# Performance work log

Hardware: AMD Instinct MI355X
Metric: run time of the kernel (lower is better)

Reference implementation:

```python
import jax, jax.numpy as jnp
import numpy as np
from jax.ops import segment_sum, segment_max

B, NPG, EPG = 2048, 32, 64          # graphs per drug, nodes/graph, edges/graph
N, E = B * NPG, B * EPG
FIN, EIN = 70, 6
HID, H, C = 128, 2, 64              # hidd_dim, conv heads, head_out_feats
NBLK, NCLASS = 4, 2
CAH, CAD = 8, 128                   # co-attention heads, dim_head


def _elu(x):
    return jnp.where(x > 0, x, jnp.expm1(x))


def _ln_graph(x, batch, w, b):
    # PyG LayerNorm(mode='graph'): normalize over all nodes+channels of each graph.
    cnt = jnp.float32(NPG * x.shape[1])  # all graphs have NPG nodes
    mean = segment_sum(x.sum(-1), batch, num_segments=B) / cnt
    xc = x - mean[batch][:, None]
    var = segment_sum((xc * xc).sum(-1), batch, num_segments=B) / cnt
    return xc * jax.lax.rsqrt(var + 1e-5)[batch][:, None] * w + b


def _ln(x, w, b):
    mu = x.mean(-1, keepdims=True)
    v = ((x - mu) ** 2).mean(-1, keepdims=True)
    return (x - mu) * jax.lax.rsqrt(v + 1e-5) * w + b


def _tconv(x, src, dst, ea, Wq, bq, Wk, bk, Wv, bv, We, Ws, bs):
    # PyG TransformerConv: edge-attention gather -> softmax over incoming edges -> scatter.
    q = (x @ Wq + bq).reshape(-1, H, C)
    k = (x @ Wk + bk).reshape(-1, H, C)
    v = (x @ Wv + bv).reshape(-1, H, C)
    e = (ea @ We).reshape(-1, H, C)
    kj = k[src] + e                                   # [E,H,C]
    a = (q[dst] * kj).sum(-1) * (C ** -0.5)           # [E,H]
    amax = segment_max(a, dst, num_segments=N)
    a = jnp.exp(a - amax[dst])
    a = a / (segment_sum(a, dst, num_segments=N)[dst] + 1e-16)
    out = segment_sum((v[src] + e) * a[:, :, None], dst, num_segments=N)
    return out.reshape(-1, H * C) + x @ Ws + bs       # root/skip connection


def _pool(x, src, dst, ea, batch, ebatch, w_rel, b_rel, w_root, W_re, b_re):
    # SAGPooling(min_score=-1): GraphConv score, per-graph softmax, all nodes kept,
    # then score-weighted global_add_pool; edge_attr pooled per graph and merged.
    agg = segment_sum(x[src], dst, num_segments=N)    # GraphConv 'add' aggregation
    score = agg @ w_rel + b_rel + x @ w_root          # [N]
    smax = segment_max(score, batch, num_segments=B)
    sexp = jnp.exp(score - smax[batch])
    score = sexp / (segment_sum(sexp, batch, num_segments=B)[batch] + 1e-16)
    g = segment_sum(x * score[:, None], batch, num_segments=B)      # [B,HID]
    ge = _elu(segment_sum(ea, ebatch, num_segments=B) @ W_re + b_re)
    g = g * ge
    return g / jnp.maximum(jnp.linalg.norm(g, axis=1, keepdims=True), 1e-12)


def _coattn(qx, kvx, lw, lb, Wq, Wkv, Wo):
    qx = _ln(qx, lw, lb)
    kvx = _ln(kvx, lw, lb)
    b, n = qx.shape[0], qx.shape[1]
    q = (qx @ Wq).reshape(b, n, CAH, CAD).transpose(0, 2, 1, 3)
    k, v = jnp.split(kvx @ Wkv, 2, axis=-1)
    k = k.reshape(b, n, CAH, CAD).transpose(0, 2, 1, 3)
    v = v.reshape(b, n, CAH, CAD).transpose(0, 2, 1, 3)
    attn = jax.nn.softmax(jnp.einsum('bhnd,bhmd->bhnm', q, k) * (CAD ** -0.5), axis=-1)
    o = jnp.einsum('bhnm,bhmd->bhnd', attn, v).transpose(0, 2, 1, 3).reshape(b, n, CAH * CAD)
    return o @ Wo


def setup_inputs() -> dict:
    key = jax.random.key(0)
    ks = iter(jax.random.split(key, 64))

    def nrm(shape, fan):
        return jax.random.normal(next(ks), shape, jnp.float32) * (fan ** -0.5)

    inp = {}
    inp['x1'] = jax.random.normal(next(ks), (N, FIN), jnp.float32)
    inp['x2'] = jax.random.normal(next(ks), (N, FIN), jnp.float32)
    inp['ea1'] = jax.random.normal(next(ks), (E, EIN), jnp.float32)
    inp['ea2'] = jax.random.normal(next(ks), (E, EIN), jnp.float32)
    inp['W_node'] = nrm((FIN, HID), FIN); inp['b_node'] = jnp.zeros((HID,), jnp.float32)
    inp['W_edge'] = nrm((EIN, 64), EIN); inp['b_edge'] = jnp.zeros((64,), jnp.float32)
    inp['ln0_w'] = jnp.ones((HID,), jnp.float32); inp['ln0_b'] = jnp.zeros((HID,), jnp.float32)
    inp['Wq'] = nrm((NBLK, 2, HID, HID), HID); inp['bq'] = jnp.zeros((NBLK, 2, HID), jnp.float32)
    inp['Wk'] = nrm((NBLK, 2, HID, HID), HID); inp['bk'] = jnp.zeros((NBLK, 2, HID), jnp.float32)
    inp['Wv'] = nrm((NBLK, 2, HID, HID), HID); inp['bv'] = jnp.zeros((NBLK, 2, HID), jnp.float32)
    inp['We'] = nrm((NBLK, 2, 64, HID), 64)
    inp['Ws'] = nrm((NBLK, 2, HID, HID), HID); inp['bs'] = jnp.zeros((NBLK, 2, HID), jnp.float32)
    inp['Wup'] = nrm((NBLK, 2, 64, 64), 64); inp['bup'] = jnp.zeros((NBLK, 2, 64), jnp.float32)
    inp['lnw'] = jnp.ones((NBLK, 2, HID), jnp.float32); inp['lnb'] = jnp.zeros((NBLK, 2, HID), jnp.float32)
    inp['w_rel'] = nrm((HID,), HID); inp['b_rel'] = jnp.zeros((), jnp.float32)
    inp['w_root'] = nrm((HID,), HID)
    inp['W_re'] = nrm((64, HID), 64); inp['b_re'] = jnp.zeros((HID,), jnp.float32)
    inp['ca_lw'] = jnp.ones((HID,), jnp.float32); inp['ca_lb'] = jnp.zeros((HID,), jnp.float32)
    inp['Wq_ca'] = nrm((HID, CAH * CAD), HID)
    inp['Wkv_ca'] = nrm((HID, 2 * CAH * CAD), HID)
    inp['Wo_ca'] = nrm((CAH * CAD, HID), CAH * CAD)
    inp['W_merge'] = nrm((NBLK * NBLK, NCLASS), NBLK * NBLK)
    inp['b_merge'] = jnp.zeros((NCLASS,), jnp.float32)
    off = jnp.repeat(jnp.arange(B, dtype=jnp.int32) * NPG, EPG)
    inp['edge_index1'] = jax.random.randint(next(ks), (2, E), 0, NPG, jnp.int32) + off[None, :]
    inp['edge_index2'] = jax.random.randint(next(ks), (2, E), 0, NPG, jnp.int32) + off[None, :]
    inp['batch1'] = jnp.repeat(jnp.arange(B, dtype=jnp.int32), NPG)
    inp['batch2'] = jnp.repeat(jnp.arange(B, dtype=jnp.int32), NPG)
    inp['ebatch1'] = jnp.repeat(jnp.arange(B, dtype=jnp.int32), EPG)
    inp['ebatch2'] = jnp.repeat(jnp.arange(B, dtype=jnp.int32), EPG)
    return inp


def reference(x1, x2, ea1, ea2, W_node, b_node, W_edge, b_edge, ln0_w, ln0_b,
              Wq, bq, Wk, bk, Wv, bv, We, Ws, bs, Wup, bup, lnw, lnb,
              w_rel, b_rel, w_root, W_re, b_re, ca_lw, ca_lb, Wq_ca, Wkv_ca, Wo_ca,
              W_merge, b_merge, edge_index1, edge_index2, batch1, batch2, ebatch1, ebatch2):
    s1, d1 = edge_index1[0], edge_index1[1]
    s2, d2 = edge_index2[0], edge_index2[1]
    x1 = _elu(_ln_graph(x1 @ W_node + b_node, batch1, ln0_w, ln0_b))
    x2 = _elu(_ln_graph(x2 @ W_node + b_node, batch2, ln0_w, ln0_b))
    ea1 = _elu(ea1 @ W_edge + b_edge)
    ea2 = _elu(ea2 @ W_edge + b_edge)

    def block(i, x, ea, src, dst, batch):
        x = _tconv(x, src, dst, ea, Wq[i, 0], bq[i, 0], Wk[i, 0], bk[i, 0],
                   Wv[i, 0], bv[i, 0], We[i, 0], Ws[i, 0], bs[i, 0])
        x = _elu(_ln_graph(x, batch, lnw[i, 0], lnb[i, 0]))
        ea = _elu(ea @ Wup[i, 0] + bup[i, 0])
        x = _tconv(x, src, dst, ea, Wq[i, 1], bq[i, 1], Wk[i, 1], bk[i, 1],
                   Wv[i, 1], bv[i, 1], We[i, 1], Ws[i, 1], bs[i, 1])
        ea_next = ea @ Wup[i, 1] + bup[i, 1]
        x = _elu(_ln_graph(x, batch, lnw[i, 1], lnb[i, 1]))
        return x, _elu(ea_next)

    hs, ts = [], []
    for i in range(NBLK):
        x1, ea1 = block(i, x1, ea1, s1, d1, batch1)
        x2, ea2 = block(i, x2, ea2, s2, d2, batch2)
        hs.append(_pool(x1, s1, d1, ea1, batch1, ebatch1, w_rel, b_rel, w_root, W_re, b_re))
        ts.append(_pool(x2, s2, d2, ea2, batch2, ebatch2, w_rel, b_rel, w_root, W_re, b_re))
    rh = jnp.stack(hs, 1)  # [B, NBLK, HID]
    rt = jnp.stack(ts, 1)
    ha = _coattn(rh, rt, ca_lw, ca_lb, Wq_ca, Wkv_ca, Wo_ca)
    ta = _coattn(rt, rh, ca_lw, ca_lb, Wq_ca, Wkv_ca, Wo_ca)
    m = jnp.einsum('bnd,bmd->bnm', ha, ta).reshape(ha.shape[0], NBLK * NBLK)
    return jax.nn.softmax(m @ W_merge + b_merge, axis=-1)
```

## Files before the change

kernel.cpp:

```cpp
#include <hip/hip_runtime.h>
#include <cstddef>
#include <cstdint>

#define NGRAPH 2048
#define NPG    32
#define EPG    64
#define NNODE  (NGRAPH*NPG)
#define NEDGE  (NGRAPH*EPG)
#define FINDIM 70
#define EINDIM 6
#define HID    128
#define NBLK   4
#define CAH    8
#define CAD    128
#define ES     68
#define XS     132

typedef __attribute__((ext_vector_type(8))) short bf16x8_t;
typedef __attribute__((ext_vector_type(4))) float f32x4;
typedef unsigned short ushortb;

#define MF3(accv, Ah_, Al_, Bh_, Bl_)                                          \
  accv = __builtin_amdgcn_mfma_f32_16x16x32_bf16(Ah_, Bh_, accv, 0, 0, 0);     \
  accv = __builtin_amdgcn_mfma_f32_16x16x32_bf16(Ah_, Bl_, accv, 0, 0, 0);     \
  accv = __builtin_amdgcn_mfma_f32_16x16x32_bf16(Al_, Bh_, accv, 0, 0, 0);

__device__ inline void split8(const float* p, bf16x8_t& h, bf16x8_t& l) {
  float4 v0 = *(const float4*)p, v1 = *(const float4*)(p + 4);
  float vv[8] = {v0.x, v0.y, v0.z, v0.w, v1.x, v1.y, v1.z, v1.w};
#pragma unroll
  for (int j = 0; j < 8; j++) {
    unsigned u = __builtin_bit_cast(unsigned, vv[j]);
    h[j] = (short)(u >> 16);
    float r = vv[j] - __builtin_bit_cast(float, u & 0xFFFF0000u);
    l[j] = (short)(__builtin_bit_cast(unsigned, r) >> 16);
  }
}

template<bool BIAS, bool ELU>
__global__ __launch_bounds__(256) void gemm_kernel(
    const float* __restrict__ A, const float* __restrict__ W,
    const float* __restrict__ bias, float* __restrict__ C,
    int M, int K, int Nc) {
  __shared__ float As[8][64];
  __shared__ float Bs[8][65];
  const int bm = blockIdx.y * 64, bn = blockIdx.x * 64;
  const int tid = threadIdx.x;
  const int tr = tid >> 4, tc = tid & 15;
  float acc[4][4];
// ... 162 lines not shown
  const int g = blockIdx.x, t = threadIdx.x;
  const float* xg = in + (size_t)g * NPG * HID;
  float* og = out + (size_t)g * NPG * HID;
  float vals[16];
  float s = 0.f, ss = 0.f;
#pragma unroll
  for (int i = 0; i < 16; i++) {
    float v = xg[t + i * 256];
    vals[i] = v; s += v; ss += v * v;
  }
  __shared__ float ws0[4], ws1[4];
  for (int off = 32; off > 0; off >>= 1) { s += __shfl_down(s, off); ss += __shfl_down(ss, off); }
  int wid = t >> 6, lane = t & 63;
  if (lane == 0) { ws0[wid] = s; ws1[wid] = ss; }
  __syncthreads();
  if (t == 0) {
    float S = 0.f, SS = 0.f;
    for (int i = 0; i < 4; i++) { S += ws0[i]; SS += ws1[i]; }
    float mean = S / 4096.f;
    float var = SS / 4096.f - mean * mean;
    ws0[0] = mean; ws1[0] = rsqrtf(var + 1e-5f);
  }
  __syncthreads();
  float mean = ws0[0], inv = ws1[0];
#pragma unroll
  for (int i = 0; i < 16; i++) {
    int idx = t + i * 256;
    int ch = idx & 127;
    float y = (vals[i] - mean) * inv * w[ch] + b[ch];
    og[idx] = y > 0.f ? y : expm1f(y);
  }
}

template<bool POOL>
__global__ __launch_bounds__(256, 4) void mega_kernel(
    float* __restrict__ xb, float* __restrict__ ea,
    const ushortb* __restrict__ Wqkvh, const ushortb* __restrict__ Wqkvl,
    const ushortb* __restrict__ Wsh, const ushortb* __restrict__ Wsl,
    const ushortb* __restrict__ WeTh, const ushortb* __restrict__ WeTl,
    const ushortb* __restrict__ Wuph, const ushortb* __restrict__ Wupl,
    const float* __restrict__ bqkv_, const float* __restrict__ bs_,
    const float* __restrict__ bup_, const float* __restrict__ lnw_,
    const float* __restrict__ lnb_,
    const float* __restrict__ w_rel, const float* __restrict__ b_rel,
    const float* __restrict__ w_root, const float* __restrict__ W_re,
    const float* __restrict__ b_re, float* __restrict__ outp, int blk,
    const int* __restrict__ src, const int* __restrict__ dst) {
  const int g = blockIdx.x, t = threadIdx.x;
  const int lane = t & 63, w = t >> 6, l16 = lane & 15, lk = lane >> 4;
  __shared__ float el[EPG * ES];
  __shared__ float qs2[NPG * ES];
  __shared__ float ks2[NPG * ES];
  __shared__ unsigned char lists[NPG * EPG];
  __shared__ int deg_[NPG];
  __shared__ int sl[EPG], dl[EPG];
  __shared__ float alE[128];
  __shared__ float red0[NPG], red1[NPG];

  if (t < EPG) { sl[t] = src[g * EPG + t] - g * NPG; dl[t] = dst[g * EPG + t] - g * NPG; }
  if (t < NPG) {
    int c = 0;
    for (int e = 0; e < EPG; e++)
      if (dl[e] == t) lists[t * EPG + (c++)] = (unsigned char)e;
    deg_[t] = c;
  }

  bf16x8_t xh[2][4], xL[2][4];
#pragma unroll
  for (int m = 0; m < 2; m++)
#pragma unroll
    for (int kc = 0; kc < 4; kc++)
      split8(xb + ((size_t)g * NPG + m * 16 + l16) * HID + kc * 32 + lk * 8,
             xh[m][kc], xL[m][kc]);
  const float* eag = ea + ((size_t)g * EPG + w * 16 + l16) * 64;

  float accH0[8], accH1[8];
#pragma unroll
  for (int c = 0; c < 8; c++) { accH0[c] = 0.f; accH1[c] = 0.f; }

  auto proj = [&](int baseN, float* dstL) {
    f32x4 pa0 = (f32x4)0.f, pa1 = (f32x4)0.f;
#pragma unroll
    for (int kc = 0; kc < 4; kc++) {
      size_t o = (size_t)(baseN + w * 16 + l16) * HID + kc * 32 + lk * 8;
      bf16x8_t bh = *(const bf16x8_t*)(Wqkvh + o);
      bf16x8_t bl = *(const bf16x8_t*)(Wqkvl + o);
      MF3(pa0, xh[0][kc], xL[0][kc], bh, bl);
      MF3(pa1, xh[1][kc], xL[1][kc], bh, bl);
    }
    float bv = bqkv_[baseN + w * 16 + l16];
#pragma unroll
    for (int r = 0; r < 4; r++) {
      dstL[(lk * 4 + r) * ES + w * 16 + l16] = pa0[r] + bv;
      dstL[(16 + lk * 4 + r) * ES + w * 16 + l16] = pa1[r] + bv;
    }
  };

  auto head = [&](const int h, float (&acc8)[8]) {
    {
      bf16x8_t ea0h, ea0l, ea1h, ea1l;
      split8(eag + lk * 8, ea0h, ea0l);
      split8(eag + 32 + lk * 8, ea1h, ea1l);
#pragma unroll 1
      for (int n = 0; n < 4; n++) {
        f32x4 acc = (f32x4)0.f;
        size_t o0 = (size_t)(h * 64 + n * 16 + l16) * 64 + lk * 8;
        bf16x8_t bh0 = *(const bf16x8_t*)(WeTh + o0);
        bf16x8_t bl0 = *(const bf16x8_t*)(WeTl + o0);
        MF3(acc, ea0h, ea0l, bh0, bl0);
        bf16x8_t bh1 = *(const bf16x8_t*)(WeTh + o0 + 32);
        bf16x8_t bl1 = *(const bf16x8_t*)(WeTl + o0 + 32);
        MF3(acc, ea1h, ea1l, bh1, bl1);
#pragma unroll
        for (int r = 0; r < 4; r++)
          el[(w * 16 + lk * 4 + r) * ES + n * 16 + l16] = acc[r];
      }
    }
    proj(h * 64, qs2);
    proj(128 + h * 64, ks2);
    __syncthreads();
    {
      const int e2 = t >> 2, part = t & 3;
      const float* qp = qs2 + dl[e2] * ES + part * 16;
      const float* kp = ks2 + sl[e2] * ES + part * 16;
      const float* ep = el + e2 * ES + part * 16;
      float s = 0.f;
#pragma unroll
      for (int c = 0; c < 16; c += 4) {
        float4 qv = *(const float4*)(qp + c);
        float4 kv = *(const float4*)(kp + c);
        float4 ev = *(const float4*)(ep + c);
        s += qv.x * (kv.x + ev.x) + qv.y * (kv.y + ev.y) +
             qv.z * (kv.z + ev.z) + qv.w * (kv.w + ev.w);
      }
      s += __shfl_xor(s, 1);
      s += __shfl_xor(s, 2);
      if (part == 0) alE[e2] = s * 0.125f;
    }
    __syncthreads();
    f32x4 va0 = (f32x4)0.f, va1 = (f32x4)0.f;
#pragma unroll
    for (int kc = 0; kc < 4; kc++) {
      size_t o = (size_t)(256 + h * 64 + w * 16 + l16) * HID + kc * 32 + lk * 8;
      bf16x8_t bh = *(const bf16x8_t*)(Wqkvh + o);
      bf16x8_t bl = *(const bf16x8_t*)(Wqkvl + o);
      MF3(va0, xh[0][kc], xL[0][kc], bh, bl);
      MF3(va1, xh[1][kc], xL[1][kc], bh, bl);
    }
    {
      const int n = t >> 3, part = t & 7;
      float su = 0.f;
#pragma unroll 1
      for (int i = 0; i < 8; i++) {
        int e2 = part * 8 + i;
        if (dl[e2] == n) su += expf(alE[e2]);
      }
      su += __shfl_xor(su, 1);
      su += __shfl_xor(su, 2);
      su += __shfl_xor(su, 4);
      if (part == 0) red1[n] = su;
    }
    {
      float bv = bqkv_[256 + h * 64 + w * 16 + l16];
#pragma unroll
      for (int r = 0; r < 4; r++) {
        ks2[(lk * 4 + r) * ES + w * 16 + l16] = va0[r] + bv;
        ks2[(16 + lk * 4 + r) * ES + w * 16 + l16] = va1[r] + bv;
      }
    }
    __syncthreads();
    {
      const int n = t >> 3, cg = t & 7;
      const float inv = 1.f / (red1[n] + 1e-16f);
      const int dg = deg_[n];
      for (int i = 0; i < dg; i++) {
        const int e2 = lists[n * EPG + i];
        const float a = expf(alE[e2]) * inv;
        const float* vp = ks2 + sl[e2] * ES + cg * 8;
        const float* ep = el + e2 * ES + cg * 8;
        float4 v0 = *(const float4*)vp, v1 = *(const float4*)(vp + 4);
        float4 e0 = *(const float4*)ep, e1 = *(const float4*)(ep + 4);
        acc8[0] += a * (v0.x + e0.x); acc8[1] += a * (v0.y + e0.y);
        acc8[2] += a * (v0.z + e0.z); acc8[3] += a * (v0.w + e0.w);
        acc8[4] += a * (v1.x + e1.x); acc8[5] += a * (v1.y + e1.y);
        acc8[6] += a * (v1.z + e1.z); acc8[7] += a * (v1.w + e1.w);
      }
    }
    __syncthreads();
  };

  head(0, accH0);
  head(1, accH1);

  {
#pragma unroll
    for (int n = 0; n < 2; n++) {
      f32x4 sa0 = (f32x4)0.f, sa1 = (f32x4)0.f;
#pragma unroll
      for (int kc = 0; kc < 4; kc++) {
        size_t o = (size_t)(w * 32 + n * 16 + l16) * HID + kc * 32 + lk * 8;
        bf16x8_t bh = *(const bf16x8_t*)(Wsh + o);
        bf16x8_t bl = *(const bf16x8_t*)(Wsl + o);
        MF3(sa0, xh[0][kc], xL[0][kc], bh, bl);
        MF3(sa1, xh[1][kc], xL[1][kc], bh, bl);
      }
      int col = w * 32 + n * 16 + l16;
      float bv = bs_[col];
#pragma unroll
      for (int r = 0; r < 4; r++) {
        el[(lk * 4 + r) * XS + col] = sa0[r] + bv;
        el[(16 + lk * 4 + r) * XS + col] = sa1[r] + bv;
      }
    }
  }
  f32x4 ua[4];
  {
    bf16x8_t ea0h, ea0l, ea1h, ea1l;
    split8(eag + lk * 8, ea0h, ea0l);
    split8(eag + 32 + lk * 8, ea1h, ea1l);
#pragma unroll
    for (int n = 0; n < 4; n++) {
      f32x4 acc = (f32x4)0.f;
      size_t o0 = (size_t)(n * 16 + l16) * 64 + lk * 8;
      bf16x8_t bh0 = *(const bf16x8_t*)(Wuph + o0);
      bf16x8_t bl0 = *(const bf16x8_t*)(Wupl + o0);
      MF3(acc, ea0h, ea0l, bh0, bl0);
      bf16x8_t bh1 = *(const bf16x8_t*)(Wuph + o0 + 32);
      bf16x8_t bl1 = *(const bf16x8_t*)(Wupl + o0 + 32);
      MF3(acc, ea1h, ea1l, bh1, bl1);
      int col = n * 16 + l16;
      float bv = bup_[col];
#pragma unroll
      for (int r = 0; r < 4; r++) {
        float y = acc[r] + bv;
        y = y > 0.f ? y : expm1f(y);
        ua[n][r] = y;
        ea[((size_t)g * EPG + w * 16 + lk * 4 + r) * 64 + col] = y;
      }
    }
  }
  __syncthreads();
  {
    const int n = t >> 3, cg = t & 7;
    float v16[16];
#pragma unroll
    for (int c = 0; c < 8; c++) {
      v16[c] = accH0[c] + el[n * XS + cg * 8 + c];
      v16[8 + c] = accH1[c] + el[n * XS + 64 + cg * 8 + c];
    }
    float s = 0.f, ss = 0.f;
#pragma unroll
    for (int j = 0; j < 16; j++) { s += v16[j]; ss += v16[j] * v16[j]; }
    for (int o2 = 32; o2 > 0; o2 >>= 1) { s += __shfl_down(s, o2); ss += __shfl_down(ss, o2); }
    if (lane == 0) { red0[w] = s; red1[w] = ss; }
    __syncthreads();
    if (t == 0) {
      float S = red0[0] + red0[1] + red0[2] + red0[3];
      float SS = red1[0] + red1[1] + red1[2] + red1[3];
      float mean = S / 4096.f;
      float var = SS / 4096.f - mean * mean;
      red0[0] = mean; red1[0] = rsqrtf(var + 1e-5f);
    }
    __syncthreads();
    float mean = red0[0], inv = red1[0];
    float* xg = xb + (size_t)g * NPG * HID;
#pragma unroll
    for (int hh = 0; hh < 2; hh++)
#pragma unroll
      for (int c = 0; c < 8; c++) {
        int col = hh * 64 + cg * 8 + c;
        float y = (v16[hh * 8 + c] - mean) * inv * lnw_[col] + lnb_[col];
        y = y > 0.f ? y : expm1f(y);
        xg[n * HID + col] = y;
        el[n * XS + col] = y;
      }
  }

  if constexpr (POOL) {
    __syncthreads();
    {
#pragma unroll
      for (int n = 0; n < 4; n++) {
        float s = ua[n][0] + ua[n][1] + ua[n][2] + ua[n][3];
        s += __shfl_xor(s, 16);
        s += __shfl_xor(s, 32);
        if (lk == 0) qs2[w * 64 + n * 16 + l16] = s;
      }
      const int n = t >> 3, part = t & 7;
      float s = 0.f;
      for (int c = part * 16; c < part * 16 + 16; c++)
        s += el[n * XS + c] * w_root[c];
      const int dg = deg_[n];
      for (int i = 0; i < dg; i++) {
        int sn = sl[lists[n * EPG + i]];
        for (int c = part * 16; c < part * 16 + 16; c++)
          s += el[sn * XS + c] * w_rel[c];
      }
      s += __shfl_xor(s, 1);
      s += __shfl_xor(s, 2);
      s += __shfl_xor(s, 4);
      if (part == 0) alE[n] = s + b_rel[0];
    }
    __syncthreads();
    if (t < 64)
      alE[64 + t] = qs2[t] + qs2[64 + t] + qs2[128 + t] + qs2[192 + t];
    if (t >= 128 && t < 160) {
      int n = t - 128;
      float sc = alE[n];
      float m = sc;
      for (int o2 = 1; o2 <= 16; o2 <<= 1) m = fmaxf(m, __shfl_xor(m, o2));
      float e = expf(sc - m);
      float su = e;
      for (int o2 = 1; o2 <= 16; o2 <<= 1) su += __shfl_xor(su, o2);
      alE[n] = e / (su + 1e-16f);
    }
    __syncthreads();
    if (t < HID) {
      const int ch = t;
      float gv = 0.f;
      for (int n = 0; n < NPG; n++) gv += alE[n] * el[n * XS + ch];
      float s2 = b_re[ch];
      for (int k2 = 0; k2 < 64; k2++) s2 += alE[64 + k2] * W_re[k2 * HID + ch];
      s2 = s2 > 0.f ? s2 : expm1f(s2);
      float gl = gv * s2;
      el[4224 + ch] = gl;
      float sq = gl * gl;
      for (int o2 = 32; o2 > 0; o2 >>= 1) sq += __shfl_down(sq, o2);
      if (lane == 0) red0[w] = sq;
    }
    __syncthreads();
    if (t == 0) red1[0] = fmaxf(sqrtf(red0[0] + red0[1]), 1e-12f);
    __syncthreads();
    if (t < HID)
      outp[((size_t)g * NBLK + blk) * HID + t] = el[4224 + t] / red1[0];
  }
}

__global__ void ln_row_kernel(const float* __restrict__ in, float* __restrict__ out,
                              const float* __restrict__ w, const float* __restrict__ b) {
  const int r = blockIdx.x, t = threadIdx.x;
  float v = in[(size_t)r * HID + t];
  float s = v, ss = v * v;
  for (int off = 32; off > 0; off >>= 1) { s += __shfl_down(s, off); ss += __shfl_down(ss, off); }
  __shared__ float s0[2], s1[2];
  if ((t & 63) == 0) { s0[t >> 6] = s; s1[t >> 6] = ss; }
  __syncthreads();
  float S = s0[0] + s0[1], SS = s1[0] + s1[1];
  float mean = S / 128.f, var = SS / 128.f - mean * mean;
  out[(size_t)r * HID + t] = (v - mean) * rsqrtf(var + 1e-5f) * w[t] + b[t];
}

__global__ void coattn_kernel(const float* __restrict__ qb, const float* __restrict__ kvb,
                              float* __restrict__ ob) {
  const int bh = blockIdx.x, b = bh >> 3, h = bh & 7, t = threadIdx.x;
  __shared__ float attn[4][4];
  __shared__ float red[64];
  const int pair = t >> 2, part = t & 3;
  const int n = pair >> 2, m = pair & 3;
  const float* qp = qb + ((size_t)(b * 4 + n) * (CAH * CAD)) + h * CAD;
  const float* kp = kvb + ((size_t)(b * 4 + m) * (2 * CAH * CAD)) + h * CAD;
  float s = 0.f;
  for (int d = part * 32; d < part * 32 + 32; d++) s += qp[d] * kp[d];
  red[t] = s;
  __syncthreads();
  if (t < 16) {
    float sc = (red[t * 4] + red[t * 4 + 1] + red[t * 4 + 2] + red[t * 4 + 3]) * 0.08838834764831845f;
    attn[t >> 2][t & 3] = sc;
// ... 110 lines not shown
  ushortb* Wkvh = allocb(262144);    ushortb* Wkvl = allocb(262144);
  ushortb* Woh = allocb(131072);     ushortb* Wol = allocb(131072);
  float* bqkv = alloc(8 * 384);
  if (off > ws_size) return;

  float* qc  = xb;
  float* kvc = big;
  float* oc  = ea;

  auto convw = [&](const float* s, ushortb* h, ushortb* l, int K, int N, int B,
                   int dstN, int nOff) {
    int tot = B * K * N;
    convw_kernel<<<(tot + 255) / 256, 256, 0, stream>>>(s, h, l, K, N, tot, dstN, nOff);
  };
  convw(Wq, Wqkvh, Wqkvl, 128, 128, 8, 384, 0);
  convw(Wk, Wqkvh, Wqkvl, 128, 128, 8, 384, 128);
  convw(Wv, Wqkvh, Wqkvl, 128, 128, 8, 384, 256);
  convw(Wskip, Wsh, Wsl, 128, 128, 8, 128, 0);
  convw(Wup, Wuph, Wupl, 64, 64, 8, 64, 0);
  convw(We, WeTh, WeTl, 64, 128, 8, 128, 0);
  convw(Wq_ca, Wqcah, Wqcal, 128, 1024, 1, 1024, 0);
  convw(Wkv_ca, Wkvh, Wkvl, 128, 2048, 1, 2048, 0);
  convw(Wo_ca, Woh, Wol, 1024, 128, 1, 128, 0);
  bcat_kernel<<<(8 * 384 + 255) / 256, 256, 0, stream>>>(bq, bk, bv, bqkv);

  for (int d2 = 0; d2 < 2; ++d2) {
    const int* src = ei[d2];
    const int* dst = ei[d2] + NEDGE;
    run_gemm(xin[d2], W_node, b_node, xb, NNODE, FINDIM, HID, false, stream);
    ln_graph_elu_kernel<<<NGRAPH, 256, 0, stream>>>(xb, xb, ln0_w, ln0_b);
    run_gemm(eain[d2], W_edge, b_edge, ea, NEDGE, EINDIM, 64, true, stream);
    float* outp = d2 == 0 ? hs : ts;
    for (int i = 0; i < NBLK; ++i) {
      int pi0 = i * 2, pi1 = i * 2 + 1;
      mega_kernel<false><<<NGRAPH, 256, 0, stream>>>(
          xb, ea,
          Wqkvh + (size_t)pi0 * 49152, Wqkvl + (size_t)pi0 * 49152,
          Wsh + (size_t)pi0 * 16384, Wsl + (size_t)pi0 * 16384,
          WeTh + (size_t)pi0 * 8192, WeTl + (size_t)pi0 * 8192,
          Wuph + (size_t)pi0 * 4096, Wupl + (size_t)pi0 * 4096,
          bqkv + pi0 * 384, bs + pi0 * 128, bup + pi0 * 64,
          lnw + pi0 * 128, lnb + pi0 * 128,
          w_rel, b_rel, w_root, W_re, b_re, nullptr, 0, src, dst);
      mega_kernel<true><<<NGRAPH, 256, 0, stream>>>(
          xb, ea,
          Wqkvh + (size_t)pi1 * 49152, Wqkvl + (size_t)pi1 * 49152,
          Wsh + (size_t)pi1 * 16384, Wsl + (size_t)pi1 * 16384,
          WeTh + (size_t)pi1 * 8192, WeTl + (size_t)pi1 * 8192,
          Wuph + (size_t)pi1 * 4096, Wupl + (size_t)pi1 * 4096,
          bqkv + pi1 * 384, bs + pi1 * 128, bup + pi1 * 64,
          lnw + pi1 * 128, lnb + pi1 * 128,
          w_rel, b_rel, w_root, W_re, b_re, outp, i, src, dst);
    }
  }

  ln_row_kernel<<<NGRAPH * NBLK, 128, 0, stream>>>(hs, rhn, ca_lw, ca_lb);
  ln_row_kernel<<<NGRAPH * NBLK, 128, 0, stream>>>(ts, rtn, ca_lw, ca_lb);
  run_mf8(rhn, Wqcah, Wqcal, qc, NGRAPH * NBLK, 128, 1024, stream);
  run_mf8(rtn, Wkvh, Wkvl, kvc, NGRAPH * NBLK, 128, 2048, stream);
  coattn_kernel<<<NGRAPH * CAH, 64, 0, stream>>>(qc, kvc, oc);
  run_mf8(oc, Woh, Wol, hab, NGRAPH * NBLK, 1024, 128, stream);
  run_mf8(rtn, Wqcah, Wqcal, qc, NGRAPH * NBLK, 128, 1024, stream);
  run_mf8(rhn, Wkvh, Wkvl, kvc, NGRAPH * NBLK, 128, 2048, stream);
  coattn_kernel<<<NGRAPH * CAH, 64, 0, stream>>>(qc, kvc, oc);
  run_mf8(oc, Woh, Wol, tab, NGRAPH * NBLK, 1024, 128, stream);

  final_kernel<<<NGRAPH, 64, 0, stream>>>(hab, tab, W_merge, b_merge, out);
}
```

Before: 3.234 ms.

## Fuse both TransformerConv layers of each block into one per-graph kernel

Merges the two per-layer mega kernels of a block into a single launch that loops over both layers. The intermediate node features and updated edge features stay in shared memory and registers between layers instead of being written to and re-read from global memory. It also saves the edge-tile setup and a kernel launch per block. In exchange the kernel holds more live state and its launch bound drops from 4 to 3 blocks per CU, which may reduce occupancy.

```diff
diff --git a/kernel.cpp b/kernel.cpp
--- a/kernel.cpp
+++ b/kernel.cpp
@@ -15,6 +15,7 @@
 #define CAD    128
 #define ES     68
 #define XS     132
+#define TS     66
 
 typedef __attribute__((ext_vector_type(8))) short bf16x8_t;
 typedef __attribute__((ext_vector_type(4))) float f32x4;
@@ -243,16 +244,15 @@
   }
 }
 
-template<bool POOL>
-__global__ __launch_bounds__(256, 4) void mega_kernel(
+__global__ __launch_bounds__(256, 3) void mega2_kernel(
     float* __restrict__ xb, float* __restrict__ ea,
-    const ushortb* __restrict__ Wqkvh, const ushortb* __restrict__ Wqkvl,
-    const ushortb* __restrict__ Wsh, const ushortb* __restrict__ Wsl,
-    const ushortb* __restrict__ WeTh, const ushortb* __restrict__ WeTl,
-    const ushortb* __restrict__ Wuph, const ushortb* __restrict__ Wupl,
-    const float* __restrict__ bqkv_, const float* __restrict__ bs_,
-    const float* __restrict__ bup_, const float* __restrict__ lnw_,
-    const float* __restrict__ lnb_,
+    const ushortb* __restrict__ Wqkvh0, const ushortb* __restrict__ Wqkvl0,
+    const ushortb* __restrict__ Wsh0, const ushortb* __restrict__ Wsl0,
+    const ushortb* __restrict__ WeTh0, const ushortb* __restrict__ WeTl0,
+    const ushortb* __restrict__ Wuph0, const ushortb* __restrict__ Wupl0,
+    const float* __restrict__ bqkv0, const float* __restrict__ bs0,
+    const float* __restrict__ bup0, const float* __restrict__ lnw0,
+    const float* __restrict__ lnb0,
     const float* __restrict__ w_rel, const float* __restrict__ b_rel,
     const float* __restrict__ w_root, const float* __restrict__ W_re,
     const float* __restrict__ b_re, float* __restrict__ outp, int blk,
@@ -260,13 +260,14 @@
   const int g = blockIdx.x, t = threadIdx.x;
   const int lane = t & 63, w = t >> 6, l16 = lane & 15, lk = lane >> 4;
   __shared__ float el[EPG * ES];
-  __shared__ float qs2[NPG * ES];
-  __shared__ float ks2[NPG * ES];
+  __shared__ float qks[2 * NPG * ES];
   __shared__ unsigned char lists[NPG * EPG];
   __shared__ int deg_[NPG];
   __shared__ int sl[EPG], dl[EPG];
   __shared__ float alE[128];
   __shared__ float red0[NPG], red1[NPG];
+  float* qs2 = qks;
+  float* ks2 = qks + NPG * ES;
 
   if (t < EPG) { sl[t] = src[g * EPG + t] - g * NPG; dl[t] = dst[g * EPG + t] - g * NPG; }
   if (t < NPG) {
@@ -283,267 +284,295 @@
     for (int kc = 0; kc < 4; kc++)
       split8(xb + ((size_t)g * NPG + m * 16 + l16) * HID + kc * 32 + lk * 8,
              xh[m][kc], xL[m][kc]);
-  const float* eag = ea + ((size_t)g * EPG + w * 16 + l16) * 64;
-
-  float accH0[8], accH1[8];
-#pragma unroll
-  for (int c = 0; c < 8; c++) { accH0[c] = 0.f; accH1[c] = 0.f; }
-
-  auto proj = [&](int baseN, float* dstL) {
-    f32x4 pa0 = (f32x4)0.f, pa1 = (f32x4)0.f;
-#pragma unroll
-    for (int kc = 0; kc < 4; kc++) {
-      size_t o = (size_t)(baseN + w * 16 + l16) * HID + kc * 32 + lk * 8;
-      bf16x8_t bh = *(const bf16x8_t*)(Wqkvh + o);
-      bf16x8_t bl = *(const bf16x8_t*)(Wqkvl + o);
-      MF3(pa0, xh[0][kc], xL[0][kc], bh, bl);
-      MF3(pa1, xh[1][kc], xL[1][kc], bh, bl);
-    }
-    float bv = bqkv_[baseN + w * 16 + l16];
-#pragma unroll
-    for (int r = 0; r < 4; r++) {
-      dstL[(lk * 4 + r) * ES + w * 16 + l16] = pa0[r] + bv;
-      dstL[(16 + lk * 4 + r) * ES + w * 16 + l16] = pa1[r] + bv;
-    }
-  };
-
-  auto head = [&](const int h, float (&acc8)[8]) {
+  bf16x8_t efh[2], efl[2];
+  {
+    const float* eag = ea + ((size_t)g * EPG + w * 16 + l16) * 64;
+    split8(eag + lk * 8, efh[0], efl[0]);
+    split8(eag + 32 + lk * 8, efh[1], efl[1]);
+  }
+
+  for (int half = 0; half < 2; ++half) {
+    const ushortb* Wqkvh = Wqkvh0 + half * 49152;
+    const ushortb* Wqkvl = Wqkvl0 + half * 49152;
+    const ushortb* Wsh = Wsh0 + half * 16384;
+    const ushortb* Wsl = Wsl0 + half * 16384;
+    const ushortb* WeTh = WeTh0 + half * 8192;
+    const ushortb* WeTl = WeTl0 + half * 8192;
+    const ushortb* Wuph = Wuph0 + half * 4096;
+    const ushortb* Wupl = Wupl0 + half * 4096;
+    const float* bqkv_ = bqkv0 + half * 384;
+    const float* bs_ = bs0 + half * 128;
+    const float* bup_ = bup0 + half * 64;
+    const float* lnw_ = lnw0 + half * 128;
+    const float* lnb_ = lnb0 + half * 128;
+
+    float accH0[8], accH1[8];
+#pragma unroll
+    for (int c = 0; c < 8; c++) { accH0[c] = 0.f; accH1[c] = 0.f; }
+
+    auto proj = [&](int baseN, float* dstL) {
+      f32x4 pa0 = (f32x4)0.f, pa1 = (f32x4)0.f;
+#pragma unroll
+      for (int kc = 0; kc < 4; kc++) {
+        size_t o = (size_t)(baseN + w * 16 + l16) * HID + kc * 32 + lk * 8;
+        bf16x8_t bh = *(const bf16x8_t*)(Wqkvh + o);
+        bf16x8_t bl = *(const bf16x8_t*)(Wqkvl + o);
+        MF3(pa0, xh[0][kc], xL[0][kc], bh, bl);
+        MF3(pa1, xh[1][kc], xL[1][kc], bh, bl);
+      }
+      float bv = bqkv_[baseN + w * 16 + l16];
+#pragma unroll
+      for (int r = 0; r < 4; r++) {
+        dstL[(lk * 4 + r) * ES + w * 16 + l16] = pa0[r] + bv;
+        dstL[(16 + lk * 4 + r) * ES + w * 16 + l16] = pa1[r] + bv;
+      }
+    };
+
+    auto head = [&](const int h, float (&acc8)[8]) {
+      {
+#pragma unroll 1
+        for (int n = 0; n < 4; n++) {
+          f32x4 acc = (f32x4)0.f;
+          size_t o0 = (size_t)(h * 64 + n * 16 + l16) * 64 + lk * 8;
+          bf16x8_t bh0 = *(const bf16x8_t*)(WeTh + o0);
+          bf16x8_t bl0 = *(const bf16x8_t*)(WeTl + o0);
+          MF3(acc, efh[0], efl[0], bh0, bl0);
+          bf16x8_t bh1 = *(const bf16x8_t*)(WeTh + o0 + 32);
+          bf16x8_t bl1 = *(const bf16x8_t*)(WeTl + o0 + 32);
+          MF3(acc, efh[1], efl[1], bh1, bl1);
+#pragma unroll
+          for (int r = 0; r < 4; r++)
+            el[(w * 16 + lk * 4 + r) * ES + n * 16 + l16] = acc[r];
+        }
+      }
+      proj(h * 64, qs2);
+      proj(128 + h * 64, ks2);
+      __syncthreads();
+      {
+        const int e2 = t >> 2, part = t & 3;
+        const float* qp = qs2 + dl[e2] * ES + part * 16;
+        const float* kp = ks2 + sl[e2] * ES + part * 16;
+        const float* ep = el + e2 * ES + part * 16;
+        float s = 0.f;
+#pragma unroll
+        for (int c = 0; c < 16; c += 4) {
+          float4 qv = *(const float4*)(qp + c);
+          float4 kv = *(const float4*)(kp + c);
+          float4 ev = *(const float4*)(ep + c);
+          s += qv.x * (kv.x + ev.x) + qv.y * (kv.y + ev.y) +
+               qv.z * (kv.z + ev.z) + qv.w * (kv.w + ev.w);
+        }
+        s += __shfl_xor(s, 1);
+        s += __shfl_xor(s, 2);
+        if (part == 0) alE[e2] = s * 0.125f;
+      }
+      __syncthreads();
+      f32x4 va0 = (f32x4)0.f, va1 = (f32x4)0.f;
+#pragma unroll
+      for (int kc = 0; kc < 4; kc++) {
+        size_t o = (size_t)(256 + h * 64 + w * 16 + l16) * HID + kc * 32 + lk * 8;
+        bf16x8_t bh = *(const bf16x8_t*)(Wqkvh + o);
+        bf16x8_t bl = *(const bf16x8_t*)(Wqkvl + o);
+        MF3(va0, xh[0][kc], xL[0][kc], bh, bl);
+        MF3(va1, xh[1][kc], xL[1][kc], bh, bl);
+      }
+      {
+        const int n = t >> 3, part = t & 7;
+        float su = 0.f;
+#pragma unroll 1
+        for (int i = 0; i < 8; i++) {
+          int e2 = part * 8 + i;
+          if (dl[e2] == n) su += expf(alE[e2]);
+        }
+        su += __shfl_xor(su, 1);
+        su += __shfl_xor(su, 2);
+        su += __shfl_xor(su, 4);
+        if (part == 0) red1[n] = su;
+      }
+      {
+        float bv = bqkv_[256 + h * 64 + w * 16 + l16];
+#pragma unroll
+        for (int r = 0; r < 4; r++) {
+          ks2[(lk * 4 + r) * ES + w * 16 + l16] = va0[r] + bv;
+          ks2[(16 + lk * 4 + r) * ES + w * 16 + l16] = va1[r] + bv;
+        }
+      }
+      __syncthreads();
+      {
+        const int n = t >> 3, cg = t & 7;
+        const float inv = 1.f / (red1[n] + 1e-16f);
+        const int dg = deg_[n];
+        for (int i = 0; i < dg; i++) {
+          const int e2 = lists[n * EPG + i];
+          const float a = expf(alE[e2]) * inv;
+          const float* vp = ks2 + sl[e2] * ES + cg * 8;
+          const float* ep = el + e2 * ES + cg * 8;
+          float4 v0 = *(const float4*)vp, v1 = *(const float4*)(vp + 4);
+          float4 e0 = *(const float4*)ep, e1 = *(const float4*)(ep + 4);
+          acc8[0] += a * (v0.x + e0.x); acc8[1] += a * (v0.y + e0.y);
+          acc8[2] += a * (v0.z + e0.z); acc8[3] += a * (v0.w + e0.w);
+          acc8[4] += a * (v1.x + e1.x); acc8[5] += a * (v1.y + e1.y);
+          acc8[6] += a * (v1.z + e1.z); acc8[7] += a * (v1.w + e1.w);
+        }
+      }
+      __syncthreads();
+    };
+
+    head(0, accH0);
+    head(1, accH1);
+
     {
-      bf16x8_t ea0h, ea0l, ea1h, ea1l;
-      split8(eag + lk * 8, ea0h, ea0l);
-      split8(eag + 32 + lk * 8, ea1h, ea1l);
-#pragma unroll 1
+#pragma unroll
+      for (int n = 0; n < 2; n++) {
+        f32x4 sa0 = (f32x4)0.f, sa1 = (f32x4)0.f;
+#pragma unroll
+        for (int kc = 0; kc < 4; kc++) {
+          size_t o = (size_t)(w * 32 + n * 16 + l16) * HID + kc * 32 + lk * 8;
+          bf16x8_t bh = *(const bf16x8_t*)(Wsh + o);
+          bf16x8_t bl = *(const bf16x8_t*)(Wsl + o);
+          MF3(sa0, xh[0][kc], xL[0][kc], bh, bl);
+          MF3(sa1, xh[1][kc], xL[1][kc], bh, bl);
+        }
+        int col = w * 32 + n * 16 + l16;
+        float bv = bs_[col];
+#pragma unroll
+        for (int r = 0; r < 4; r++) {
+          el[(lk * 4 + r) * XS + col] = sa0[r] + bv;
+          el[(16 + lk * 4 + r) * XS + col] = sa1[r] + bv;
+        }
+      }
+    }
+    f32x4 ua[4];
+    {
+#pragma unroll
       for (int n = 0; n < 4; n++) {
         f32x4 acc = (f32x4)0.f;
-        size_t o0 = (size_t)(h * 64 + n * 16 + l16) * 64 + lk * 8;
-        bf16x8_t bh0 = *(const bf16x8_t*)(WeTh + o0);
-        bf16x8_t bl0 = *(const bf16x8_t*)(WeTl + o0);
-        MF3(acc, ea0h, ea0l, bh0, bl0);
-        bf16x8_t bh1 = *(const bf16x8_t*)(WeTh + o0 + 32);
-        bf16x8_t bl1 = *(const bf16x8_t*)(WeTl + o0 + 32);
-        MF3(acc, ea1h, ea1l, bh1, bl1);
-#pragma unroll
-        for (int r = 0; r < 4; r++)
-          el[(w * 16 + lk * 4 + r) * ES + n * 16 + l16] = acc[r];
-      }
-    }
-    proj(h * 64, qs2);
-    proj(128 + h * 64, ks2);
-    __syncthreads();
-    {
-      const int e2 = t >> 2, part = t & 3;
-      const float* qp = qs2 + dl[e2] * ES + part * 16;
-      const float* kp = ks2 + sl[e2] * ES + part * 16;
-      const float* ep = el + e2 * ES + part * 16;
-      float s = 0.f;
-#pragma unroll
-      for (int c = 0; c < 16; c += 4) {
-        float4 qv = *(const float4*)(qp + c);
-        float4 kv = *(const float4*)(kp + c);
-        float4 ev = *(const float4*)(ep + c);
-        s += qv.x * (kv.x + ev.x) + qv.y * (kv.y + ev.y) +
-             qv.z * (kv.z + ev.z) + qv.w * (kv.w + ev.w);
-      }
-      s += __shfl_xor(s, 1);
-      s += __shfl_xor(s, 2);
-      if (part == 0) alE[e2] = s * 0.125f;
-    }
-    __syncthreads();
-    f32x4 va0 = (f32x4)0.f, va1 = (f32x4)0.f;
-#pragma unroll
-    for (int kc = 0; kc < 4; kc++) {
-      size_t o = (size_t)(256 + h * 64 + w * 16 + l16) * HID + kc * 32 + lk * 8;
-      bf16x8_t bh = *(const bf16x8_t*)(Wqkvh + o);
-      bf16x8_t bl = *(const bf16x8_t*)(Wqkvl + o);
-      MF3(va0, xh[0][kc], xL[0][kc], bh, bl);
-      MF3(va1, xh[1][kc], xL[1][kc], bh, bl);
-    }
-    {
-      const int n = t >> 3, part = t & 7;
-      float su = 0.f;
-#pragma unroll 1
-      for (int i = 0; i < 8; i++) {
-        int e2 = part * 8 + i;
-        if (dl[e2] == n) su += expf(alE[e2]);
-      }
-      su += __shfl_xor(su, 1);
-      su += __shfl_xor(su, 2);
-      su += __shfl_xor(su, 4);
-      if (part == 0) red1[n] = su;
-    }
-    {
-      float bv = bqkv_[256 + h * 64 + w * 16 + l16];
-#pragma unroll
-      for (int r = 0; r < 4; r++) {
-        ks2[(lk * 4 + r) * ES + w * 16 + l16] = va0[r] + bv;
-        ks2[(16 + lk * 4 + r) * ES + w * 16 + l16] = va1[r] + bv;
+        size_t o0 = (size_t)(n * 16 + l16) * 64 + lk * 8;
+        bf16x8_t bh0 = *(const bf16x8_t*)(Wuph + o0);
+        bf16x8_t bl0 = *(const bf16x8_t*)(Wupl + o0);
+        MF3(acc, efh[0], efl[0], bh0, bl0);
+        bf16x8_t bh1 = *(const bf16x8_t*)(Wuph + o0 + 32);
+        bf16x8_t bl1 = *(const bf16x8_t*)(Wupl + o0 + 32);
+        MF3(acc, efh[1], efl[1], bh1, bl1);
+        int col = n * 16 + l16;
+        float bv = bup_[col];
+#pragma unroll
+        for (int r = 0; r < 4; r++) {
+          float y = acc[r] + bv;
+          y = y > 0.f ? y : expm1f(y);
+          ua[n][r] = y;
+          if (half == 0)
+            qks[(w * 16 + lk * 4 + r) * TS + col] = y;
+          else
+            ea[((size_t)g * EPG + w * 16 + lk * 4 + r) * 64 + col] = y;
+        }
       }
     }
     __syncthreads();
     {
       const int n = t >> 3, cg = t & 7;
-      const float inv = 1.f / (red1[n] + 1e-16f);
-      const int dg = deg_[n];
-      for (int i = 0; i < dg; i++) {
-        const int e2 = lists[n * EPG + i];
-        const float a = expf(alE[e2]) * inv;
-        const float* vp = ks2 + sl[e2] * ES + cg * 8;
-        const float* ep = el + e2 * ES + cg * 8;
-        float4 v0 = *(const float4*)vp, v1 = *(const float4*)(vp + 4);
-        float4 e0 = *(const float4*)ep, e1 = *(const float4*)(ep + 4);
-        acc8[0] += a * (v0.x + e0.x); acc8[1] += a * (v0.y + e0.y);
-        acc8[2] += a * (v0.z + e0.z); acc8[3] += a * (v0.w + e0.w);
-        acc8[4] += a * (v1.x + e1.x); acc8[5] += a * (v1.y + e1.y);
-        acc8[6] += a * (v1.z + e1.z); acc8[7] += a * (v1.w + e1.w);
-      }
-    }
-    __syncthreads();
-  };
-
-  head(0, accH0);
-  head(1, accH1);
-
-  {
-#pragma unroll
-    for (int n = 0; n < 2; n++) {
-      f32x4 sa0 = (f32x4)0.f, sa1 = (f32x4)0.f;
-#pragma unroll
-      for (int kc = 0; kc < 4; kc++) {
-        size_t o = (size_t)(w * 32 + n * 16 + l16) * HID + kc * 32 + lk * 8;
-        bf16x8_t bh = *(const bf16x8_t*)(Wsh + o);
-        bf16x8_t bl = *(const bf16x8_t*)(Wsl + o);
-        MF3(sa0, xh[0][kc], xL[0][kc], bh, bl);
-        MF3(sa1, xh[1][kc], xL[1][kc], bh, bl);
-      }
-      int col = w * 32 + n * 16 + l16;
-      float bv = bs_[col];
-#pragma unroll
-      for (int r = 0; r < 4; r++) {
-        el[(lk * 4 + r) * XS + col] = sa0[r] + bv;
-        el[(16 + lk * 4 + r) * XS + col] = sa1[r] + bv;
-      }
-    }
-  }
-  f32x4 ua[4];
-  {
-    bf16x8_t ea0h, ea0l, ea1h, ea1l;
-    split8(eag + lk * 8, ea0h, ea0l);
-    split8(eag + 32 + lk * 8, ea1h, ea1l);
-#pragma unroll
-    for (int n = 0; n < 4; n++) {
-      f32x4 acc = (f32x4)0.f;
-      size_t o0 = (size_t)(n * 16 + l16) * 64 + lk * 8;
-      bf16x8_t bh0 = *(const bf16x8_t*)(Wuph + o0);
-      bf16x8_t bl0 = *(const bf16x8_t*)(Wupl + o0);
-      MF3(acc, ea0h, ea0l, bh0, bl0);
-      bf16x8_t bh1 = *(const bf16x8_t*)(Wuph + o0 + 32);
-      bf16x8_t bl1 = *(const bf16x8_t*)(Wupl + o0 + 32);
-      MF3(acc, ea1h, ea1l, bh1, bl1);
-      int col = n * 16 + l16;
-      float bv = bup_[col];
-#pragma unroll
-      for (int r = 0; r < 4; r++) {
-        float y = acc[r] + bv;
-        y = y > 0.f ? y : expm1f(y);
-        ua[n][r] = y;
-        ea[((size_t)g * EPG + w * 16 + lk * 4 + r) * 64 + col] = y;
-      }
-    }
-  }
-  __syncthreads();
-  {
-    const int n = t >> 3, cg = t & 7;
-    float v16[16];
-#pragma unroll
-    for (int c = 0; c < 8; c++) {
-      v16[c] = accH0[c] + el[n * XS + cg * 8 + c];
-      v16[8 + c] = accH1[c] + el[n * XS + 64 + cg * 8 + c];
-    }
-    float s = 0.f, ss = 0.f;
-#pragma unroll
-    for (int j = 0; j < 16; j++) { s += v16[j]; ss += v16[j] * v16[j]; }
-    for (int o2 = 32; o2 > 0; o2 >>= 1) { s += __shfl_down(s, o2); ss += __shfl_down(ss, o2); }
-    if (lane == 0) { red0[w] = s; red1[w] = ss; }
-    __syncthreads();
-    if (t == 0) {
-      float S = red0[0] + red0[1] + red0[2] + red0[3];
-      float SS = red1[0] + red1[1] + red1[2] + red1[3];
-      float mean = S / 4096.f;
-      float var = SS / 4096.f - mean * mean;
-      red0[0] = mean; red1[0] = rsqrtf(var + 1e-5f);
-    }
-    __syncthreads();
-    float mean = red0[0], inv = red1[0];
-    float* xg = xb + (size_t)g * NPG * HID;
-#pragma unroll
-    for (int hh = 0; hh < 2; hh++)
+      float v16[16];
 #pragma unroll
       for (int c = 0; c < 8; c++) {
-        int col = hh * 64 + cg * 8 + c;
-        float y = (v16[hh * 8 + c] - mean) * inv * lnw_[col] + lnb_[col];
-        y = y > 0.f ? y : expm1f(y);
-        xg[n * HID + col] = y;
-        el[n * XS + col] = y;
-      }
-  }
-
-  if constexpr (POOL) {
-    __syncthreads();
-    {
-#pragma unroll
-      for (int n = 0; n < 4; n++) {
-        float s = ua[n][0] + ua[n][1] + ua[n][2] + ua[n][3];
-        s += __shfl_xor(s, 16);
-        s += __shfl_xor(s, 32);
-        if (lk == 0) qs2[w * 64 + n * 16 + l16] = s;
-      }
-      const int n = t >> 3, part = t & 7;
-      float s = 0.f;
-      for (int c = part * 16; c < part * 16 + 16; c++)
-        s += el[n * XS + c] * w_root[c];
-      const int dg = deg_[n];
-      for (int i = 0; i < dg; i++) {
-        int sn = sl[lists[n * EPG + i]];
+        v16[c] = accH0[c] + el[n * XS + cg * 8 + c];
+        v16[8 + c] = accH1[c] + el[n * XS + 64 + cg * 8 + c];
+      }
+      float s = 0.f, ss = 0.f;
+#pragma unroll
+      for (int j = 0; j < 16; j++) { s += v16[j]; ss += v16[j] * v16[j]; }
+      for (int o2 = 32; o2 > 0; o2 >>= 1) { s += __shfl_down(s, o2); ss += __shfl_down(ss, o2); }
+      if (lane == 0) { red0[w] = s; red1[w] = ss; }
+      __syncthreads();
+      if (t == 0) {
+        float S = red0[0] + red0[1] + red0[2] + red0[3];
+        float SS = red1[0] + red1[1] + red1[2] + red1[3];
+        float mean = S / 4096.f;
+        float var = SS / 4096.f - mean * mean;
+        red0[0] = mean; red1[0] = rsqrtf(var + 1e-5f);
+      }
+      __syncthreads();
+      float mean = red0[0], inv = red1[0];
+      float* xg = xb + (size_t)g * NPG * HID;
+#pragma unroll
+      for (int hh = 0; hh < 2; hh++)
+#pragma unroll
+        for (int c = 0; c < 8; c++) {
+          int col = hh * 64 + cg * 8 + c;
+          float y = (v16[hh * 8 + c] - mean) * inv * lnw_[col] + lnb_[col];
+          y = y > 0.f ? y : expm1f(y);
+          if (half == 1) xg[n * HID + col] = y;
+          el[n * XS + col] = y;
+        }
+    }
+
+    if (half == 0) {
+      __syncthreads();
+#pragma unroll
+      for (int m = 0; m < 2; m++)
+#pragma unroll
+        for (int kc = 0; kc < 4; kc++)
+          split8(&el[(m * 16 + l16) * XS + kc * 32 + lk * 8], xh[m][kc], xL[m][kc]);
+      split8(&qks[(w * 16 + l16) * TS + lk * 8], efh[0], efl[0]);
+      split8(&qks[(w * 16 + l16) * TS + 32 + lk * 8], efh[1], efl[1]);
+      __syncthreads();
+    } else {
+      __syncthreads();
+      {
+#pragma unroll
+        for (int n = 0; n < 4; n++) {
+          float s = ua[n][0] + ua[n][1] + ua[n][2] + ua[n][3];
+          s += __shfl_xor(s, 16);
+          s += __shfl_xor(s, 32);
+          if (lk == 0) qs2[w * 64 + n * 16 + l16] = s;
+        }
+        const int n = t >> 3, part = t & 7;
+        float s = 0.f;
         for (int c = part * 16; c < part * 16 + 16; c++)
-          s += el[sn * XS + c] * w_rel[c];
-      }
-      s += __shfl_xor(s, 1);
-      s += __shfl_xor(s, 2);
-      s += __shfl_xor(s, 4);
-      if (part == 0) alE[n] = s + b_rel[0];
-    }
-    __syncthreads();
-    if (t < 64)
-      alE[64 + t] = qs2[t] + qs2[64 + t] + qs2[128 + t] + qs2[192 + t];
-    if (t >= 128 && t < 160) {
-      int n = t - 128;
-      float sc = alE[n];
-      float m = sc;
-      for (int o2 = 1; o2 <= 16; o2 <<= 1) m = fmaxf(m, __shfl_xor(m, o2));
-      float e = expf(sc - m);
-      float su = e;
-      for (int o2 = 1; o2 <= 16; o2 <<= 1) su += __shfl_xor(su, o2);
-      alE[n] = e / (su + 1e-16f);
-    }
-    __syncthreads();
-    if (t < HID) {
-      const int ch = t;
-      float gv = 0.f;
-      for (int n = 0; n < NPG; n++) gv += alE[n] * el[n * XS + ch];
-      float s2 = b_re[ch];
-      for (int k2 = 0; k2 < 64; k2++) s2 += alE[64 + k2] * W_re[k2 * HID + ch];
-      s2 = s2 > 0.f ? s2 : expm1f(s2);
-      float gl = gv * s2;
-      el[4224 + ch] = gl;
-      float sq = gl * gl;
-      for (int o2 = 32; o2 > 0; o2 >>= 1) sq += __shfl_down(sq, o2);
-      if (lane == 0) red0[w] = sq;
-    }
-    __syncthreads();
-    if (t == 0) red1[0] = fmaxf(sqrtf(red0[0] + red0[1]), 1e-12f);
-    __syncthreads();
-    if (t < HID)
-      outp[((size_t)g * NBLK + blk) * HID + t] = el[4224 + t] / red1[0];
+          s += el[n * XS + c] * w_root[c];
+        const int dg = deg_[n];
+        for (int i = 0; i < dg; i++) {
+          int sn = sl[lists[n * EPG + i]];
+          for (int c = part * 16; c < part * 16 + 16; c++)
+            s += el[sn * XS + c] * w_rel[c];
+        }
+        s += __shfl_xor(s, 1);
+        s += __shfl_xor(s, 2);
+        s += __shfl_xor(s, 4);
+        if (part == 0) alE[n] = s + b_rel[0];
+      }
+      __syncthreads();
+      if (t < 64)
+        alE[64 + t] = qs2[t] + qs2[64 + t] + qs2[128 + t] + qs2[192 + t];
+      if (t >= 128 && t < 160) {
+        int n = t - 128;
+        float sc = alE[n];
+        float m = sc;
+        for (int o2 = 1; o2 <= 16; o2 <<= 1) m = fmaxf(m, __shfl_xor(m, o2));
+        float e = expf(sc - m);
+        float su = e;
+        for (int o2 = 1; o2 <= 16; o2 <<= 1) su += __shfl_xor(su, o2);
+        alE[n] = e / (su + 1e-16f);
+      }
+      __syncthreads();
+      if (t < HID) {
+        const int ch = t;
+        float gv = 0.f;
+        for (int n = 0; n < NPG; n++) gv += alE[n] * el[n * XS + ch];
+        float s2 = b_re[ch];
+        for (int k2 = 0; k2 < 64; k2++) s2 += alE[64 + k2] * W_re[k2 * HID + ch];
+        s2 = s2 > 0.f ? s2 : expm1f(s2);
+        float gl = gv * s2;
+        el[4224 + ch] = gl;
+        float sq = gl * gl;
+        for (int o2 = 32; o2 > 0; o2 >>= 1) sq += __shfl_down(sq, o2);
+        if (lane == 0) red0[w] = sq;
+      }
+      __syncthreads();
+      if (t == 0) red1[0] = fmaxf(sqrtf(red0[0] + red0[1]), 1e-12f);
+      __syncthreads();
+      if (t < HID)
+        outp[((size_t)g * NBLK + blk) * HID + t] = el[4224 + t] / red1[0];
+    }
   }
 }
 
@@ -720,8 +749,8 @@
     run_gemm(eain[d2], W_edge, b_edge, ea, NEDGE, EINDIM, 64, true, stream);
     float* outp = d2 == 0 ? hs : ts;
     for (int i = 0; i < NBLK; ++i) {
-      int pi0 = i * 2, pi1 = i * 2 + 1;
-      mega_kernel<false><<<NGRAPH, 256, 0, stream>>>(
+      int pi0 = i * 2;
+      mega2_kernel<<<NGRAPH, 256, 0, stream>>>(
           xb, ea,
           Wqkvh + (size_t)pi0 * 49152, Wqkvl + (size_t)pi0 * 49152,
           Wsh + (size_t)pi0 * 16384, Wsl + (size_t)pi0 * 16384,
@@ -729,15 +758,6 @@
           Wuph + (size_t)pi0 * 4096, Wupl + (size_t)pi0 * 4096,
           bqkv + pi0 * 384, bs + pi0 * 128, bup + pi0 * 64,
           lnw + pi0 * 128, lnb + pi0 * 128,
-          w_rel, b_rel, w_root, W_re, b_re, nullptr, 0, src, dst);
-      mega_kernel<true><<<NGRAPH, 256, 0, stream>>>(
-          xb, ea,
-          Wqkvh + (size_t)pi1 * 49152, Wqkvl + (size_t)pi1 * 49152,
-          Wsh + (size_t)pi1 * 16384, Wsl + (size_t)pi1 * 16384,
-          WeTh + (size_t)pi1 * 8192, WeTl + (size_t)pi1 * 8192,
-          Wuph + (size_t)pi1 * 4096, Wupl + (size_t)pi1 * 4096,
-          bqkv + pi1 * 384, bs + pi1 * 128, bup + pi1 * 64,
-          lnw + pi1 * 128, lnb + pi1 * 128,
           w_rel, b_rel, w_root, W_re, b_re, outp, i, src, dst);
     }
   }
```

Result: slower. 4.516 ms (+39.6%).

## Split node rows across wave pairs to halve per-wave x fragment registers

Applied to the files above, without the earlier changes.

Each wave now holds only 16 of the 32 node rows of the split-bf16 x fragments, selected by wave parity, instead of all 32. Column tiles for the QKV, V and skip projections are redistributed so that each wave pair covers the full column range. This halves the x-fragment register footprint, which may relieve register pressure and spilling under launch_bounds(256,4). The cost is that each wave now loads twice as many weight fragments per MFMA, so weight traffic from cache roughly doubles.

```diff
diff --git a/kernel.cpp b/kernel.cpp
--- a/kernel.cpp
+++ b/kernel.cpp
@@ -259,6 +259,7 @@
     const int* __restrict__ src, const int* __restrict__ dst) {
   const int g = blockIdx.x, t = threadIdx.x;
   const int lane = t & 63, w = t >> 6, l16 = lane & 15, lk = lane >> 4;
+  const int mh = w & 1, cp = w >> 1;
   __shared__ float el[EPG * ES];
   __shared__ float qs2[NPG * ES];
   __shared__ float ks2[NPG * ES];
@@ -276,13 +277,11 @@
     deg_[t] = c;
   }
 
-  bf16x8_t xh[2][4], xL[2][4];
-#pragma unroll
-  for (int m = 0; m < 2; m++)
-#pragma unroll
-    for (int kc = 0; kc < 4; kc++)
-      split8(xb + ((size_t)g * NPG + m * 16 + l16) * HID + kc * 32 + lk * 8,
-             xh[m][kc], xL[m][kc]);
+  bf16x8_t xh[4], xL[4];
+#pragma unroll
+  for (int kc = 0; kc < 4; kc++)
+    split8(xb + ((size_t)g * NPG + mh * 16 + l16) * HID + kc * 32 + lk * 8,
+           xh[kc], xL[kc]);
   const float* eag = ea + ((size_t)g * EPG + w * 16 + l16) * 64;
 
   float accH0[8], accH1[8];
@@ -290,20 +289,21 @@
   for (int c = 0; c < 8; c++) { accH0[c] = 0.f; accH1[c] = 0.f; }
 
   auto proj = [&](int baseN, float* dstL) {
-    f32x4 pa0 = (f32x4)0.f, pa1 = (f32x4)0.f;
-#pragma unroll
-    for (int kc = 0; kc < 4; kc++) {
-      size_t o = (size_t)(baseN + w * 16 + l16) * HID + kc * 32 + lk * 8;
-      bf16x8_t bh = *(const bf16x8_t*)(Wqkvh + o);
-      bf16x8_t bl = *(const bf16x8_t*)(Wqkvl + o);
-      MF3(pa0, xh[0][kc], xL[0][kc], bh, bl);
-      MF3(pa1, xh[1][kc], xL[1][kc], bh, bl);
-    }
-    float bv = bqkv_[baseN + w * 16 + l16];
-#pragma unroll
-    for (int r = 0; r < 4; r++) {
-      dstL[(lk * 4 + r) * ES + w * 16 + l16] = pa0[r] + bv;
-      dstL[(16 + lk * 4 + r) * ES + w * 16 + l16] = pa1[r] + bv;
+#pragma unroll
+    for (int ct = 0; ct < 2; ct++) {
+      const int col0 = cp * 32 + ct * 16;
+      f32x4 pa = (f32x4)0.f;
+#pragma unroll
+      for (int kc = 0; kc < 4; kc++) {
+        size_t o = (size_t)(baseN + col0 + l16) * HID + kc * 32 + lk * 8;
+        bf16x8_t bh = *(const bf16x8_t*)(Wqkvh + o);
+        bf16x8_t bl = *(const bf16x8_t*)(Wqkvl + o);
+        MF3(pa, xh[kc], xL[kc], bh, bl);
+      }
+      float bv = bqkv_[baseN + col0 + l16];
+#pragma unroll
+      for (int r = 0; r < 4; r++)
+        dstL[(mh * 16 + lk * 4 + r) * ES + col0 + l16] = pa[r] + bv;
     }
   };
 
@@ -349,14 +349,18 @@
       if (part == 0) alE[e2] = s * 0.125f;
     }
     __syncthreads();
-    f32x4 va0 = (f32x4)0.f, va1 = (f32x4)0.f;
-#pragma unroll
-    for (int kc = 0; kc < 4; kc++) {
-      size_t o = (size_t)(256 + h * 64 + w * 16 + l16) * HID + kc * 32 + lk * 8;
-      bf16x8_t bh = *(const bf16x8_t*)(Wqkvh + o);
-      bf16x8_t bl = *(const bf16x8_t*)(Wqkvl + o);
-      MF3(va0, xh[0][kc], xL[0][kc], bh, bl);
-      MF3(va1, xh[1][kc], xL[1][kc], bh, bl);
+    f32x4 va[2];
+#pragma unroll
+    for (int ct = 0; ct < 2; ct++) {
+      const int col0 = cp * 32 + ct * 16;
+      va[ct] = (f32x4)0.f;
+#pragma unroll
+      for (int kc = 0; kc < 4; kc++) {
+        size_t o = (size_t)(256 + h * 64 + col0 + l16) * HID + kc * 32 + lk * 8;
+        bf16x8_t bh = *(const bf16x8_t*)(Wqkvh + o);
+        bf16x8_t bl = *(const bf16x8_t*)(Wqkvl + o);
+        MF3(va[ct], xh[kc], xL[kc], bh, bl);
+      }
     }
     {
       const int n = t >> 3, part = t & 7;
@@ -372,11 +376,13 @@
       if (part == 0) red1[n] = su;
     }
     {
-      float bv = bqkv_[256 + h * 64 + w * 16 + l16];
-#pragma unroll
-      for (int r = 0; r < 4; r++) {
-        ks2[(lk * 4 + r) * ES + w * 16 + l16] = va0[r] + bv;
-        ks2[(16 + lk * 4 + r) * ES + w * 16 + l16] = va1[r] + bv;
+#pragma unroll
+      for (int ct = 0; ct < 2; ct++) {
+        const int col0 = cp * 32 + ct * 16;
+        float bv = bqkv_[256 + h * 64 + col0 + l16];
+#pragma unroll
+        for (int r = 0; r < 4; r++)
+          ks2[(mh * 16 + lk * 4 + r) * ES + col0 + l16] = va[ct][r] + bv;
       }
     }
     __syncthreads();
@@ -405,23 +411,20 @@
 
   {
 #pragma unroll
-    for (int n = 0; n < 2; n++) {
-      f32x4 sa0 = (f32x4)0.f, sa1 = (f32x4)0.f;
+    for (int ct = 0; ct < 4; ct++) {
+      const int col0 = cp * 64 + ct * 16;
+      f32x4 sa = (f32x4)0.f;
 #pragma unroll
       for (int kc = 0; kc < 4; kc++) {
-        size_t o = (size_t)(w * 32 + n * 16 + l16) * HID + kc * 32 + lk * 8;
+        size_t o = (size_t)(col0 + l16) * HID + kc * 32 + lk * 8;
         bf16x8_t bh = *(const bf16x8_t*)(Wsh + o);
         bf16x8_t bl = *(const bf16x8_t*)(Wsl + o);
-        MF3(sa0, xh[0][kc], xL[0][kc], bh, bl);
-        MF3(sa1, xh[1][kc], xL[1][kc], bh, bl);
-      }
-      int col = w * 32 + n * 16 + l16;
-      float bv = bs_[col];
-#pragma unroll
-      for (int r = 0; r < 4; r++) {
-        el[(lk * 4 + r) * XS + col] = sa0[r] + bv;
-        el[(16 + lk * 4 + r) * XS + col] = sa1[r] + bv;
-      }
+        MF3(sa, xh[kc], xL[kc], bh, bl);
+      }
+      float bv = bs_[col0 + l16];
+#pragma unroll
+      for (int r = 0; r < 4; r++)
+        el[(mh * 16 + lk * 4 + r) * XS + col0 + l16] = sa[r] + bv;
     }
   }
   f32x4 ua[4];
```

After: 3.914 ms. 1.21x slower.
